# Optimization experiments

Measured on AMD Instinct MI355X. Metric: run time of the kernel, lower is better.

## Reference

```python
import jax, jax.numpy as jnp
import numpy as np

B, T, D = 32, 8192, 256
CTX = 128

def setup_inputs() -> dict:
    key = jax.random.key(0)
    kx, kw, ku = jax.random.split(key, 3)
    X = jax.random.normal(kx, (B, T, D), dtype=jnp.float32)
    # keras 'uniform' initializer: U(-0.05, 0.05)
    W = jax.random.uniform(kw, (D, CTX), dtype=jnp.float32, minval=-0.05, maxval=0.05)
    u = jax.random.uniform(ku, (CTX, 1), dtype=jnp.float32, minval=-0.05, maxval=0.05)
    return {"X": X, "W": W, "u": u}

def reference(X, W, u):
    # additive attention over time axis
    u_tw = jnp.tanh(jnp.einsum('btd,dc->btc', X, W))        # (B,T,CTX)
    scores = jnp.einsum('btc,co->bt', u_tw, u)              # (B,T)
    att = jax.nn.softmax(scores, axis=1)                    # (B,T)
    # weighted sum over time, no repeated-elements materialization
    return jnp.einsum('bt,btd->bd', att, X)                 # (B,D)
```

## Files before the change

kernel.cpp:

```cpp
#include <hip/hip_runtime.h>
#include <stdint.h>

#define B_N   32
#define T_N   8192
#define D_N   256
#define CTX_N 128
#define TB    32
#define CPB   8
#define ROWS_PB (TB*CPB)
#define BLK_PER_B (T_N/ROWS_PB)
#define NBLOCKS (B_N*BLK_PER_B)
#define XP    264
#define SPW   12

typedef unsigned short u16;
typedef unsigned int   u32;
typedef __attribute__((ext_vector_type(8))) short bf16x8;
typedef __attribute__((ext_vector_type(8))) unsigned short u16x8;
typedef __attribute__((ext_vector_type(4))) float f32x4;

__device__ __forceinline__ u16 f2bf(float f) {
  u32 u = __float_as_uint(f);
  return (u16)((u + 0x7FFFu + ((u >> 16) & 1u)) >> 16);
}
__device__ __forceinline__ float bf2f(u16 h) {
  return __uint_as_float(((u32)h) << 16);
}
__device__ __forceinline__ float fast_tanh(float x) {
  float e = __expf(2.0f * x);
  return (e - 1.0f) * __builtin_amdgcn_rcpf(e + 1.0f);
}
__device__ __forceinline__ float rr16_add(float v) {
  int x;
  x = __builtin_amdgcn_update_dpp(0, __float_as_int(v), 0x128, 0xF, 0xF, true); v += __int_as_float(x);
  x = __builtin_amdgcn_update_dpp(0, __float_as_int(v), 0x124, 0xF, 0xF, true); v += __int_as_float(x);
  x = __builtin_amdgcn_update_dpp(0, __float_as_int(v), 0x122, 0xF, 0xF, true); v += __int_as_float(x);
  x = __builtin_amdgcn_update_dpp(0, __float_as_int(v), 0x121, 0xF, 0xF, true); v += __int_as_float(x);
  return v;
}

__global__ void prep_w(const float* __restrict__ W, u16* __restrict__ Wt) {
  int c = blockIdx.x;
  int d = threadIdx.x;
  Wt[c * D_N + d] = f2bf(W[d * CTX_N + c]);
}

__global__ __launch_bounds__(512, 4)
void attn_main(const float* __restrict__ X, const u16* __restrict__ Wt,
               const float* __restrict__ u,
               float* __restrict__ blk_o, float* __restrict__ blk_l) {
  __shared__ u16   Xl[3][TB][XP];
  __shared__ __align__(16) float s_part[2][TB][SPW];
  __shared__ float l_part[16];

  const int tid = threadIdx.x;
  const int w   = tid >> 6;
  const int l   = tid & 63;
  const int l15 = l & 15;
  const int lg  = l >> 4;

  const int blk  = blockIdx.x;
  const int b    = blk >> 5;
  const int rowB = (blk & (BLK_PER_B - 1)) * ROWS_PB;
  const float* Xbase = X + ((size_t)b * T_N + rowB) * D_N;

  bf16x8 bw[8];
  {
    const u16* wp = Wt + (w * 16 + l15) * D_N + lg * 8;
    #pragma unroll
    for (int kk = 0; kk < 8; ++kk) bw[kk] = *(const bf16x8*)(wp + kk * 32);
  }
  const float uc = u[w * 16 + l15];

  const int srow = tid >> 4;
  const int scol = (tid & 15) << 4;

  float4 pf0, pf1, pf2, pf3;
  {
    const float* sp = Xbase + (size_t)srow * D_N + scol;
    pf0 = ((const float4*)sp)[0]; pf1 = ((const float4*)sp)[1];
    pf2 = ((const float4*)sp)[2]; pf3 = ((const float4*)sp)[3];
  }

  const int g     = tid >> 5;
  const int slice = tid & 31;
  float o8[8] = {0,0,0,0,0,0,0,0};
  float l_run = 0.f;

  auto wsum = [&](int m) {
    const int pb = m % 3, sp = m & 1;
    float4 sa0 = *(const float4*)&s_part[sp][2 * g][0];
    float4 sa1 = *(const float4*)&s_part[sp][2 * g][4];
    float4 sb0 = *(const float4*)&s_part[sp][2 * g + 1][0];
    float4 sb1 = *(const float4*)&s_part[sp][2 * g + 1][4];
    float st0 = sa0.x; st0 += sa0.y; st0 += sa0.z; st0 += sa0.w;
    st0 += sa1.x; st0 += sa1.y; st0 += sa1.z; st0 += sa1.w;
    float st1 = sb0.x; st1 += sb0.y; st1 += sb0.z; st1 += sb0.w;
    st1 += sb1.x; st1 += sb1.y; st1 += sb1.z; st1 += sb1.w;
    float p0 = __expf(st0), p1 = __expf(st1);
    if (slice == 0) l_run += p0 + p1;
    u16x8 x0 = *(const u16x8*)&Xl[pb][2 * g][slice * 8];
    u16x8 x1 = *(const u16x8*)&Xl[pb][2 * g + 1][slice * 8];
    #pragma unroll
    for (int j = 0; j < 8; ++j) o8[j] += p0 * bf2f(x0[j]) + p1 * bf2f(x1[j]);
  };

  for (int c = 0; c < CPB; ++c) {
    const int cb = c % 3;

    u16x8 s0, s1;
    s0[0]=f2bf(pf0.x); s0[1]=f2bf(pf0.y); s0[2]=f2bf(pf0.z); s0[3]=f2bf(pf0.w);
    s0[4]=f2bf(pf1.x); s0[5]=f2bf(pf1.y); s0[6]=f2bf(pf1.z); s0[7]=f2bf(pf1.w);
    s1[0]=f2bf(pf2.x); s1[1]=f2bf(pf2.y); s1[2]=f2bf(pf2.z); s1[3]=f2bf(pf2.w);
    s1[4]=f2bf(pf3.x); s1[5]=f2bf(pf3.y); s1[6]=f2bf(pf3.z); s1[7]=f2bf(pf3.w);
    *(u16x8*)&Xl[cb][srow][scol]     = s0;
    *(u16x8*)&Xl[cb][srow][scol + 8] = s1;

    if (c + 1 < CPB) {
      const float* sp = Xbase + ((size_t)(c + 1) * TB + srow) * D_N + scol;
      pf0 = ((const float4*)sp)[0]; pf1 = ((const float4*)sp)[1];
      pf2 = ((const float4*)sp)[2]; pf3 = ((const float4*)sp)[3];
    }

    asm volatile("s_waitcnt lgkmcnt(0)" ::: "memory");
    __builtin_amdgcn_s_barrier();
    asm volatile("" ::: "memory");

    if (c >= 1) wsum(c - 1);

    const u16* Xc = &Xl[cb][0][0];
    f32x4 acc0 = {0,0,0,0}, acc1 = {0,0,0,0};
    #pragma unroll
    for (int kk = 0; kk < 8; ++kk) {
      bf16x8 a0 = *(const bf16x8*)(Xc + l15 * XP + kk * 32 + lg * 8);
      bf16x8 a1 = *(const bf16x8*)(Xc + (16 + l15) * XP + kk * 32 + lg * 8);
      acc0 = __builtin_amdgcn_mfma_f32_16x16x32_bf16(a0, bw[kk], acc0, 0, 0, 0);
      acc1 = __builtin_amdgcn_mfma_f32_16x16x32_bf16(a1, bw[kk], acc1, 0, 0, 0);
    }
    #pragma unroll
    for (int r = 0; r < 4; ++r) {
      float v0 = rr16_add(uc * fast_tanh(acc0[r]));
      float v1 = rr16_add(uc * fast_tanh(acc1[r]));
      if (l15 == 0) {
        s_part[c & 1][lg * 4 + r][w]      = v0;
        s_part[c & 1][16 + lg * 4 + r][w] = v1;
      }
    }
  }

  asm volatile("s_waitcnt lgkmcnt(0)" ::: "memory");
  __builtin_amdgcn_s_barrier();
  asm volatile("" ::: "memory");
  wsum(CPB - 1);

  asm volatile("s_waitcnt lgkmcnt(0)" ::: "memory");
  __builtin_amdgcn_s_barrier();
  asm volatile("" ::: "memory");
  float* comb = (float*)&Xl[0][0][0];
  #pragma unroll
  for (int j = 0; j < 8; ++j) comb[g * 256 + slice * 8 + j] = o8[j];
  if (slice == 0) l_part[g] = l_run;
  asm volatile("s_waitcnt lgkmcnt(0)" ::: "memory");
  __builtin_amdgcn_s_barrier();
  asm volatile("" ::: "memory");
  if (tid < 256) {
    float o = 0.f;
    #pragma unroll
    for (int g2 = 0; g2 < 16; ++g2) o += comb[g2 * 256 + tid];
    blk_o[(size_t)blk * D_N + tid] = o;
  }
  if (tid == 0) {
    float L = 0.f;
    #pragma unroll
    for (int g2 = 0; g2 < 16; ++g2) L += l_part[g2];
    blk_l[blk] = L;
  }
}

__global__ __launch_bounds__(256)
void finalize(const float* __restrict__ blk_o, const float* __restrict__ blk_l,
              float* __restrict__ out) {
  const int b = blockIdx.x, d = threadIdx.x;
  float o = 0.f, L = 0.f;
  for (int i = 0; i < BLK_PER_B; ++i) {
    o += blk_o[(size_t)(b * BLK_PER_B + i) * D_N + d];
    L += blk_l[b * BLK_PER_B + i];
  }
  out[b * D_N + d] = o / L;
}

extern "C" void kernel_launch(void* const* d_in, const int* in_sizes, int n_in,
                              void* d_out, int out_size, void* d_ws, size_t ws_size,
                              hipStream_t stream) {
  const float* X = (const float*)d_in[0];
  const float* W = (const float*)d_in[1];
  const float* u = (const float*)d_in[2];
  float* out = (float*)d_out;

  u16*   Wt    = (u16*)d_ws;
  float* blk_o = (float*)((char*)d_ws + 65536);
  float* blk_l = (float*)((char*)d_ws + 65536 + (size_t)NBLOCKS * D_N * 4);

  prep_w<<<CTX_N, D_N, 0, stream>>>(W, Wt);
  attn_main<<<NBLOCKS, 512, 0, stream>>>(X, Wt, u, blk_o, blk_l);
  finalize<<<B_N, 256, 0, stream>>>(blk_o, blk_l, out);
}
```

Measured before the change: 58.76 us.

## Halve block to 256 threads with each wave covering 32 context columns

The attention kernel now runs 4 waves per block instead of 8. Each wave holds two 16-column W fragments and issues four MFMAs per k-step, reusing each X fragment twice. Global X loads are remapped so each wave loads whole rows with float4 per lane, and the weighted-sum stage now processes 4 rows per thread group. The epilogue drops one barrier and uses vector stores. The change roughly doubles per-thread register use and lowers the occupancy bound, so there are fewer threads to hide memory latency on a kernel that is likely bandwidth-bound.

```diff
diff --git a/kernel.cpp b/kernel.cpp
--- a/kernel.cpp
+++ b/kernel.cpp
@@ -11,12 +11,13 @@
 #define BLK_PER_B (T_N/ROWS_PB)
 #define NBLOCKS (B_N*BLK_PER_B)
 #define XP    264
-#define SPW   12
+#define SPW   4
 
 typedef unsigned short u16;
 typedef unsigned int   u32;
 typedef __attribute__((ext_vector_type(8))) short bf16x8;
 typedef __attribute__((ext_vector_type(8))) unsigned short u16x8;
+typedef __attribute__((ext_vector_type(4))) unsigned short u16x4;
 typedef __attribute__((ext_vector_type(4))) float f32x4;
 
 __device__ __forceinline__ u16 f2bf(float f) {
@@ -45,13 +46,13 @@
   Wt[c * D_N + d] = f2bf(W[d * CTX_N + c]);
 }
 
-__global__ __launch_bounds__(512, 4)
+__global__ __launch_bounds__(256, 3)
 void attn_main(const float* __restrict__ X, const u16* __restrict__ Wt,
                const float* __restrict__ u,
                float* __restrict__ blk_o, float* __restrict__ blk_l) {
   __shared__ u16   Xl[3][TB][XP];
   __shared__ __align__(16) float s_part[2][TB][SPW];
-  __shared__ float l_part[16];
+  __shared__ float l_part[8];
 
   const int tid = threadIdx.x;
   const int w   = tid >> 6;
@@ -64,63 +65,66 @@
   const int rowB = (blk & (BLK_PER_B - 1)) * ROWS_PB;
   const float* Xbase = X + ((size_t)b * T_N + rowB) * D_N;
 
-  bf16x8 bw[8];
+  bf16x8 bw0[8], bw1[8];
   {
-    const u16* wp = Wt + (w * 16 + l15) * D_N + lg * 8;
-    #pragma unroll
-    for (int kk = 0; kk < 8; ++kk) bw[kk] = *(const bf16x8*)(wp + kk * 32);
-  }
-  const float uc = u[w * 16 + l15];
-
-  const int srow = tid >> 4;
-  const int scol = (tid & 15) << 4;
-
-  float4 pf0, pf1, pf2, pf3;
-  {
-    const float* sp = Xbase + (size_t)srow * D_N + scol;
-    pf0 = ((const float4*)sp)[0]; pf1 = ((const float4*)sp)[1];
-    pf2 = ((const float4*)sp)[2]; pf3 = ((const float4*)sp)[3];
-  }
-
-  const int g     = tid >> 5;
-  const int slice = tid & 31;
+    const u16* wp0 = Wt + (w * 32 + l15) * D_N + lg * 8;
+    const u16* wp1 = wp0 + 16 * D_N;
+    #pragma unroll
+    for (int kk = 0; kk < 8; ++kk) {
+      bw0[kk] = *(const bf16x8*)(wp0 + kk * 32);
+      bw1[kk] = *(const bf16x8*)(wp1 + kk * 32);
+    }
+  }
+  const float uc0 = u[w * 32 + l15];
+  const float uc1 = u[w * 32 + 16 + l15];
+
+  const float* Xs = Xbase + (size_t)w * D_N + (l << 2);
+
+  float4 pf0, pf1, pf2, pf3, pf4, pf5, pf6, pf7;
+#define LOADP(cn) {                                                      \
+    const float* sp_ = Xs + (size_t)(cn) * TB * D_N;                     \
+    pf0 = *(const float4*)(sp_ + 0  * D_N * 4);                          \
+    pf1 = *(const float4*)(sp_ + 1  * D_N * 4);                          \
+    pf2 = *(const float4*)(sp_ + 2  * D_N * 4);                          \
+    pf3 = *(const float4*)(sp_ + 3  * D_N * 4);                          \
+    pf4 = *(const float4*)(sp_ + 4  * D_N * 4);                          \
+    pf5 = *(const float4*)(sp_ + 5  * D_N * 4);                          \
+    pf6 = *(const float4*)(sp_ + 6  * D_N * 4);                          \
+    pf7 = *(const float4*)(sp_ + 7  * D_N * 4);                          \
+  }
+#define ST1(P, j) { u16x4 t_;                                            \
+    t_[0]=f2bf(P.x); t_[1]=f2bf(P.y); t_[2]=f2bf(P.z); t_[3]=f2bf(P.w);  \
+    *(u16x4*)&Xl[cb][4*(j) + w][l << 2] = t_; }
+
+  LOADP(0);
+
+  const int g  = tid >> 5;
+  const int sl = tid & 31;
   float o8[8] = {0,0,0,0,0,0,0,0};
   float l_run = 0.f;
 
   auto wsum = [&](int m) {
     const int pb = m % 3, sp = m & 1;
-    float4 sa0 = *(const float4*)&s_part[sp][2 * g][0];
-    float4 sa1 = *(const float4*)&s_part[sp][2 * g][4];
-    float4 sb0 = *(const float4*)&s_part[sp][2 * g + 1][0];
-    float4 sb1 = *(const float4*)&s_part[sp][2 * g + 1][4];
-    float st0 = sa0.x; st0 += sa0.y; st0 += sa0.z; st0 += sa0.w;
-    st0 += sa1.x; st0 += sa1.y; st0 += sa1.z; st0 += sa1.w;
-    float st1 = sb0.x; st1 += sb0.y; st1 += sb0.z; st1 += sb0.w;
-    st1 += sb1.x; st1 += sb1.y; st1 += sb1.z; st1 += sb1.w;
-    float p0 = __expf(st0), p1 = __expf(st1);
-    if (slice == 0) l_run += p0 + p1;
-    u16x8 x0 = *(const u16x8*)&Xl[pb][2 * g][slice * 8];
-    u16x8 x1 = *(const u16x8*)&Xl[pb][2 * g + 1][slice * 8];
-    #pragma unroll
-    for (int j = 0; j < 8; ++j) o8[j] += p0 * bf2f(x0[j]) + p1 * bf2f(x1[j]);
+    #pragma unroll
+    for (int k = 0; k < 4; ++k) {
+      const int row = 4 * g + k;
+      float4 sa = *(const float4*)&s_part[sp][row][0];
+      float st = sa.x; st += sa.y; st += sa.z; st += sa.w;
+      float p = __expf(st);
+      if (sl == 0) l_run += p;
+      u16x8 x = *(const u16x8*)&Xl[pb][row][sl * 8];
+      #pragma unroll
+      for (int j = 0; j < 8; ++j) o8[j] += p * bf2f(x[j]);
+    }
   };
 
   for (int c = 0; c < CPB; ++c) {
     const int cb = c % 3;
 
-    u16x8 s0, s1;
-    s0[0]=f2bf(pf0.x); s0[1]=f2bf(pf0.y); s0[2]=f2bf(pf0.z); s0[3]=f2bf(pf0.w);
-    s0[4]=f2bf(pf1.x); s0[5]=f2bf(pf1.y); s0[6]=f2bf(pf1.z); s0[7]=f2bf(pf1.w);
-    s1[0]=f2bf(pf2.x); s1[1]=f2bf(pf2.y); s1[2]=f2bf(pf2.z); s1[3]=f2bf(pf2.w);
-    s1[4]=f2bf(pf3.x); s1[5]=f2bf(pf3.y); s1[6]=f2bf(pf3.z); s1[7]=f2bf(pf3.w);
-    *(u16x8*)&Xl[cb][srow][scol]     = s0;
-    *(u16x8*)&Xl[cb][srow][scol + 8] = s1;
-
-    if (c + 1 < CPB) {
-      const float* sp = Xbase + ((size_t)(c + 1) * TB + srow) * D_N + scol;
-      pf0 = ((const float4*)sp)[0]; pf1 = ((const float4*)sp)[1];
-      pf2 = ((const float4*)sp)[2]; pf3 = ((const float4*)sp)[3];
-    }
+    ST1(pf0, 0) ST1(pf1, 1) ST1(pf2, 2) ST1(pf3, 3)
+    ST1(pf4, 4) ST1(pf5, 5) ST1(pf6, 6) ST1(pf7, 7)
+
+    if (c + 1 < CPB) LOADP(c + 1);
 
     asm volatile("s_waitcnt lgkmcnt(0)" ::: "memory");
     __builtin_amdgcn_s_barrier();
@@ -129,18 +133,20 @@
     if (c >= 1) wsum(c - 1);
 
     const u16* Xc = &Xl[cb][0][0];
-    f32x4 acc0 = {0,0,0,0}, acc1 = {0,0,0,0};
+    f32x4 a00 = {0,0,0,0}, a01 = {0,0,0,0}, a10 = {0,0,0,0}, a11 = {0,0,0,0};
     #pragma unroll
     for (int kk = 0; kk < 8; ++kk) {
-      bf16x8 a0 = *(const bf16x8*)(Xc + l15 * XP + kk * 32 + lg * 8);
-      bf16x8 a1 = *(const bf16x8*)(Xc + (16 + l15) * XP + kk * 32 + lg * 8);
-      acc0 = __builtin_amdgcn_mfma_f32_16x16x32_bf16(a0, bw[kk], acc0, 0, 0, 0);
-      acc1 = __builtin_amdgcn_mfma_f32_16x16x32_bf16(a1, bw[kk], acc1, 0, 0, 0);
+      bf16x8 fa0 = *(const bf16x8*)(Xc + l15 * XP + kk * 32 + lg * 8);
+      bf16x8 fa1 = *(const bf16x8*)(Xc + (16 + l15) * XP + kk * 32 + lg * 8);
+      a00 = __builtin_amdgcn_mfma_f32_16x16x32_bf16(fa0, bw0[kk], a00, 0, 0, 0);
+      a01 = __builtin_amdgcn_mfma_f32_16x16x32_bf16(fa0, bw1[kk], a01, 0, 0, 0);
+      a10 = __builtin_amdgcn_mfma_f32_16x16x32_bf16(fa1, bw0[kk], a10, 0, 0, 0);
+      a11 = __builtin_amdgcn_mfma_f32_16x16x32_bf16(fa1, bw1[kk], a11, 0, 0, 0);
     }
     #pragma unroll
     for (int r = 0; r < 4; ++r) {
-      float v0 = rr16_add(uc * fast_tanh(acc0[r]));
-      float v1 = rr16_add(uc * fast_tanh(acc1[r]));
+      float v0 = rr16_add(uc0 * fast_tanh(a00[r]) + uc1 * fast_tanh(a01[r]));
+      float v1 = rr16_add(uc0 * fast_tanh(a10[r]) + uc1 * fast_tanh(a11[r]));
       if (l15 == 0) {
         s_part[c & 1][lg * 4 + r][w]      = v0;
         s_part[c & 1][16 + lg * 4 + r][w] = v1;
@@ -153,28 +159,27 @@
   asm volatile("" ::: "memory");
   wsum(CPB - 1);
 
+  float* comb = (float*)&Xl[0][0][0];
+  *(float4*)&comb[g * 256 + sl * 8]     = *(float4*)&o8[0];
+  *(float4*)&comb[g * 256 + sl * 8 + 4] = *(float4*)&o8[4];
+  if (sl == 0) l_part[g] = l_run;
   asm volatile("s_waitcnt lgkmcnt(0)" ::: "memory");
   __builtin_amdgcn_s_barrier();
   asm volatile("" ::: "memory");
-  float* comb = (float*)&Xl[0][0][0];
-  #pragma unroll
-  for (int j = 0; j < 8; ++j) comb[g * 256 + slice * 8 + j] = o8[j];
-  if (slice == 0) l_part[g] = l_run;
-  asm volatile("s_waitcnt lgkmcnt(0)" ::: "memory");
-  __builtin_amdgcn_s_barrier();
-  asm volatile("" ::: "memory");
-  if (tid < 256) {
+  {
     float o = 0.f;
     #pragma unroll
-    for (int g2 = 0; g2 < 16; ++g2) o += comb[g2 * 256 + tid];
+    for (int g2 = 0; g2 < 8; ++g2) o += comb[g2 * 256 + tid];
     blk_o[(size_t)blk * D_N + tid] = o;
   }
   if (tid == 0) {
     float L = 0.f;
     #pragma unroll
-    for (int g2 = 0; g2 < 16; ++g2) L += l_part[g2];
+    for (int g2 = 0; g2 < 8; ++g2) L += l_part[g2];
     blk_l[blk] = L;
   }
+#undef LOADP
+#undef ST1
 }
 
 __global__ __launch_bounds__(256)
@@ -202,6 +207,6 @@
   float* blk_l = (float*)((char*)d_ws + 65536 + (size_t)NBLOCKS * D_N * 4);
 
   prep_w<<<CTX_N, D_N, 0, stream>>>(W, Wt);
-  attn_main<<<NBLOCKS, 512, 0, stream>>>(X, Wt, u, blk_o, blk_l);
+  attn_main<<<NBLOCKS, 256, 0, stream>>>(X, Wt, u, blk_o, blk_l);
   finalize<<<B_N, 256, 0, stream>>>(blk_o, blk_l, out);
 }
```

Result: slower. 73.69 us (+25.4%).

## Specialize waves: four compute MFMA scores, four do weighted sum

Applied to the files above, without the earlier changes.

Splits the 8 waves of each block by role. Waves 0-3 each compute 32 context columns with two MFMA accumulators that reuse each loaded A fragment, fusing the two tanh*u contributions before the cross-lane reduction. Waves 4-7 handle only the exp-weighted accumulation of the previous chunk. The aim is to run the MFMA and weighted-sum phases concurrently on different waves and to halve LDS A-fragment reads, at the cost of doubling the W registers held by compute waves and risking imbalance between the two roles.

```diff
diff --git a/kernel.cpp b/kernel.cpp
--- a/kernel.cpp
+++ b/kernel.cpp
@@ -11,7 +11,7 @@
 #define BLK_PER_B (T_N/ROWS_PB)
 #define NBLOCKS (B_N*BLK_PER_B)
 #define XP    264
-#define SPW   12
+#define SPW   4
 
 typedef unsigned short u16;
 typedef unsigned int   u32;
@@ -51,7 +51,7 @@
                float* __restrict__ blk_o, float* __restrict__ blk_l) {
   __shared__ u16   Xl[3][TB][XP];
   __shared__ __align__(16) float s_part[2][TB][SPW];
-  __shared__ float l_part[16];
+  __shared__ float l_part[8];
 
   const int tid = threadIdx.x;
   const int w   = tid >> 6;
@@ -64,45 +64,47 @@
   const int rowB = (blk & (BLK_PER_B - 1)) * ROWS_PB;
   const float* Xbase = X + ((size_t)b * T_N + rowB) * D_N;
 
-  bf16x8 bw[8];
-  {
-    const u16* wp = Wt + (w * 16 + l15) * D_N + lg * 8;
-    #pragma unroll
-    for (int kk = 0; kk < 8; ++kk) bw[kk] = *(const bf16x8*)(wp + kk * 32);
-  }
-  const float uc = u[w * 16 + l15];
+  bf16x8 bw0[8], bw1[8];
+  float uc0 = 0.f, uc1 = 0.f;
+  if (w < 4) {
+    const u16* wp0 = Wt + (w * 32 + l15) * D_N + lg * 8;
+    const u16* wp1 = wp0 + 16 * D_N;
+    #pragma unroll
+    for (int kk = 0; kk < 8; ++kk) {
+      bw0[kk] = *(const bf16x8*)(wp0 + kk * 32);
+      bw1[kk] = *(const bf16x8*)(wp1 + kk * 32);
+    }
+    uc0 = u[w * 32 + l15];
+    uc1 = u[w * 32 + 16 + l15];
+  }
 
   const int srow = tid >> 4;
   const int scol = (tid & 15) << 4;
+  const float* Xrow = Xbase + (size_t)srow * D_N + scol;
 
   float4 pf0, pf1, pf2, pf3;
-  {
-    const float* sp = Xbase + (size_t)srow * D_N + scol;
-    pf0 = ((const float4*)sp)[0]; pf1 = ((const float4*)sp)[1];
-    pf2 = ((const float4*)sp)[2]; pf3 = ((const float4*)sp)[3];
-  }
-
-  const int g     = tid >> 5;
-  const int slice = tid & 31;
+  pf0 = ((const float4*)Xrow)[0]; pf1 = ((const float4*)Xrow)[1];
+  pf2 = ((const float4*)Xrow)[2]; pf3 = ((const float4*)Xrow)[3];
+
+  const int hw   = w - 4;
+  const int subr = l >> 5;
+  const int sl   = l & 31;
   float o8[8] = {0,0,0,0,0,0,0,0};
   float l_run = 0.f;
 
   auto wsum = [&](int m) {
     const int pb = m % 3, sp = m & 1;
-    float4 sa0 = *(const float4*)&s_part[sp][2 * g][0];
-    float4 sa1 = *(const float4*)&s_part[sp][2 * g][4];
-    float4 sb0 = *(const float4*)&s_part[sp][2 * g + 1][0];
-    float4 sb1 = *(const float4*)&s_part[sp][2 * g + 1][4];
-    float st0 = sa0.x; st0 += sa0.y; st0 += sa0.z; st0 += sa0.w;
-    st0 += sa1.x; st0 += sa1.y; st0 += sa1.z; st0 += sa1.w;
-    float st1 = sb0.x; st1 += sb0.y; st1 += sb0.z; st1 += sb0.w;
-    st1 += sb1.x; st1 += sb1.y; st1 += sb1.z; st1 += sb1.w;
-    float p0 = __expf(st0), p1 = __expf(st1);
-    if (slice == 0) l_run += p0 + p1;
-    u16x8 x0 = *(const u16x8*)&Xl[pb][2 * g][slice * 8];
-    u16x8 x1 = *(const u16x8*)&Xl[pb][2 * g + 1][slice * 8];
-    #pragma unroll
-    for (int j = 0; j < 8; ++j) o8[j] += p0 * bf2f(x0[j]) + p1 * bf2f(x1[j]);
+    #pragma unroll
+    for (int k = 0; k < 4; ++k) {
+      const int row = hw * 8 + 2 * k + subr;
+      float4 sa = *(const float4*)&s_part[sp][row][0];
+      float st = sa.x; st += sa.y; st += sa.z; st += sa.w;
+      float p = __expf(st);
+      if (sl == 0) l_run += p;
+      u16x8 x = *(const u16x8*)&Xl[pb][row][sl * 8];
+      #pragma unroll
+      for (int j = 0; j < 8; ++j) o8[j] += p * bf2f(x[j]);
+    }
   };
 
   for (int c = 0; c < CPB; ++c) {
@@ -117,62 +119,61 @@
     *(u16x8*)&Xl[cb][srow][scol + 8] = s1;
 
     if (c + 1 < CPB) {
-      const float* sp = Xbase + ((size_t)(c + 1) * TB + srow) * D_N + scol;
-      pf0 = ((const float4*)sp)[0]; pf1 = ((const float4*)sp)[1];
-      pf2 = ((const float4*)sp)[2]; pf3 = ((const float4*)sp)[3];
+      const float* sp_ = Xrow + (size_t)(c + 1) * TB * D_N;
+      pf0 = ((const float4*)sp_)[0]; pf1 = ((const float4*)sp_)[1];
+      pf2 = ((const float4*)sp_)[2]; pf3 = ((const float4*)sp_)[3];
     }
 
     asm volatile("s_waitcnt lgkmcnt(0)" ::: "memory");
     __builtin_amdgcn_s_barrier();
     asm volatile("" ::: "memory");
 
-    if (c >= 1) wsum(c - 1);
-
-    const u16* Xc = &Xl[cb][0][0];
-    f32x4 acc0 = {0,0,0,0}, acc1 = {0,0,0,0};
-    #pragma unroll
-    for (int kk = 0; kk < 8; ++kk) {
-      bf16x8 a0 = *(const bf16x8*)(Xc + l15 * XP + kk * 32 + lg * 8);
-      bf16x8 a1 = *(const bf16x8*)(Xc + (16 + l15) * XP + kk * 32 + lg * 8);
-      acc0 = __builtin_amdgcn_mfma_f32_16x16x32_bf16(a0, bw[kk], acc0, 0, 0, 0);
-      acc1 = __builtin_amdgcn_mfma_f32_16x16x32_bf16(a1, bw[kk], acc1, 0, 0, 0);
-    }
-    #pragma unroll
-    for (int r = 0; r < 4; ++r) {
-      float v0 = rr16_add(uc * fast_tanh(acc0[r]));
-      float v1 = rr16_add(uc * fast_tanh(acc1[r]));
-      if (l15 == 0) {
-        s_part[c & 1][lg * 4 + r][w]      = v0;
-        s_part[c & 1][16 + lg * 4 + r][w] = v1;
+    if (w < 4) {
+      const u16* Xc = &Xl[cb][0][0];
+      #pragma unroll
+      for (int t = 0; t < 2; ++t) {
+        f32x4 acc0 = {0,0,0,0}, acc1 = {0,0,0,0};
+        #pragma unroll
+        for (int kk = 0; kk < 8; ++kk) {
+          bf16x8 a = *(const bf16x8*)(Xc + (t * 16 + l15) * XP + kk * 32 + lg * 8);
+          acc0 = __builtin_amdgcn_mfma_f32_16x16x32_bf16(a, bw0[kk], acc0, 0, 0, 0);
+          acc1 = __builtin_amdgcn_mfma_f32_16x16x32_bf16(a, bw1[kk], acc1, 0, 0, 0);
+        }
+        #pragma unroll
+        for (int r = 0; r < 4; ++r) {
+          float v = rr16_add(uc0 * fast_tanh(acc0[r]) + uc1 * fast_tanh(acc1[r]));
+          if (l15 == 0) s_part[c & 1][t * 16 + lg * 4 + r][w] = v;
+        }
       }
-    }
-  }
-
-  asm volatile("s_waitcnt lgkmcnt(0)" ::: "memory");
-  __builtin_amdgcn_s_barrier();
-  asm volatile("" ::: "memory");
-  wsum(CPB - 1);
+    } else {
+      if (c >= 1) wsum(c - 1);
+    }
+  }
 
   asm volatile("s_waitcnt lgkmcnt(0)" ::: "memory");
   __builtin_amdgcn_s_barrier();
   asm volatile("" ::: "memory");
   float* comb = (float*)&Xl[0][0][0];
-  #pragma unroll
-  for (int j = 0; j < 8; ++j) comb[g * 256 + slice * 8 + j] = o8[j];
-  if (slice == 0) l_part[g] = l_run;
+  if (w >= 4) {
+    wsum(CPB - 1);
+    const int q = hw * 2 + subr;
+    *(float4*)&comb[q * 256 + sl * 8]     = *(float4*)&o8[0];
+    *(float4*)&comb[q * 256 + sl * 8 + 4] = *(float4*)&o8[4];
+    if (sl == 0) l_part[q] = l_run;
+  }
   asm volatile("s_waitcnt lgkmcnt(0)" ::: "memory");
   __builtin_amdgcn_s_barrier();
   asm volatile("" ::: "memory");
   if (tid < 256) {
     float o = 0.f;
     #pragma unroll
-    for (int g2 = 0; g2 < 16; ++g2) o += comb[g2 * 256 + tid];
+    for (int q2 = 0; q2 < 8; ++q2) o += comb[q2 * 256 + tid];
     blk_o[(size_t)blk * D_N + tid] = o;
   }
   if (tid == 0) {
     float L = 0.f;
     #pragma unroll
-    for (int g2 = 0; g2 < 16; ++g2) L += l_part[g2];
+    for (int q2 = 0; q2 < 8; ++q2) L += l_part[q2];
     blk_l[blk] = L;
   }
 }
```

New measurement: 61.44 us. 1.05x slower.
